# Performance work log

Hardware: AMD Instinct MI355X
Metric: run time of the kernel (lower is better)

## Reference

```python
import jax, jax.numpy as jnp
import numpy as np

V, E, H, T, B, L = 50000, 256, 256, 20, 64, 512
START, STOP = 18, 19
NEG = -10000.0


def setup_inputs() -> dict:
    key = jax.random.key(0)
    ks = jax.random.split(key, 16)
    lengths = jnp.sort(jax.random.randint(ks[0], (B,), 1, L + 1))[::-1]
    lengths = lengths.at[0].set(L)  # pack_padded requires sorted descending
    sentences = jax.random.randint(ks[1], (B, L), 0, V)
    s = lambda k, shp, sc: jax.random.normal(k, shp, jnp.float32) * sc
    trans = jax.random.normal(ks[12], (T, T), jnp.float32)
    trans = trans.at[START, :].set(NEG).at[:, STOP].set(NEG)
    return {
        "sentences": sentences,
        "lengths": lengths,
        "emb": s(ks[2], (V, E), 1.0),
        "w_ih_f": s(ks[3], (4 * H, E), 0.05),
        "w_hh_f": s(ks[4], (4 * H, H), 0.05),
        "b_ih_f": s(ks[5], (4 * H,), 0.05),
        "b_hh_f": s(ks[6], (4 * H,), 0.05),
        "w_ih_b": s(ks[7], (4 * H, E), 0.05),
        "w_hh_b": s(ks[8], (4 * H, H), 0.05),
        "b_ih_b": s(ks[9], (4 * H,), 0.05),
        "b_hh_b": s(ks[10], (4 * H,), 0.05),
        "w_out": s(ks[11], (T, 2 * H), 0.05),
        "b_out": s(ks[13], (T,), 0.05),
        "transitions": trans,
    }


def _lstm(x, mask, w_ih, w_hh, b_ih, b_hh):
    # x: [B,L,E]; mask: [B,L] bool. Masked scan == packed-sequence LSTM
    # (hidden frozen past length, outputs zero past length like pad_packed).
    h0 = jnp.zeros((x.shape[0], H), x.dtype)
    bias = b_ih + b_hh

    def step(carry, inp):
        h, c = carry
        xt, mt = inp
        g = xt @ w_ih.T + h @ w_hh.T + bias
        i, f, gg, o = jnp.split(g, 4, axis=-1)  # torch gate order i,f,g,o
        c_new = jax.nn.sigmoid(f) * c + jax.nn.sigmoid(i) * jnp.tanh(gg)
        h_new = jax.nn.sigmoid(o) * jnp.tanh(c_new)
        m = mt[:, None]
        h = jnp.where(m, h_new, h)
        c = jnp.where(m, c_new, c)
        return (h, c), jnp.where(m, h_new, 0.0)

    _, hs = jax.lax.scan(step, (h0, h0), (x.transpose(1, 0, 2), mask.T))
    return hs.transpose(1, 0, 2)  # [B,L,H]


def _emissions(sentences, lengths, emb, w_ih_f, w_hh_f, b_ih_f, b_hh_f,
               w_ih_b, w_hh_b, b_ih_b, b_hh_b, w_out, b_out):
    mask = jnp.arange(L)[None, :] < lengths[:, None]  # [B,L]
    embeds = emb[sentences]  # [B,L,E]
    out_f = _lstm(embeds, mask, w_ih_f, w_hh_f, b_ih_f, b_hh_f)
    # backward dir: reverse each sequence within its own length
    rev_idx = jnp.clip(lengths[:, None] - 1 - jnp.arange(L)[None, :], 0, L - 1)
    x_rev = jnp.take_along_axis(embeds, rev_idx[:, :, None], axis=1)
    h_rev = _lstm(x_rev, mask, w_ih_b, w_hh_b, b_ih_b, b_hh_b)
    out_b = jnp.take_along_axis(h_rev, rev_idx[:, :, None], axis=1) * mask[..., None]
    lstm_out = jnp.concatenate([out_f, out_b], axis=-1)  # [B,L,2H]
    return lstm_out @ w_out.T + b_out  # [B,L,T]


def _viterbi(scores, lengths, transitions):
    mask = jnp.arange(L)[None, :] < lengths[:, None]
    fv0 = jnp.full((B, T), NEG, scores.dtype).at[:, START].set(0.0)

    def step(fv, inp):
        sc_t, m_t = inp  # [B,T], [B]
        ntv = fv[:, None, :] + transitions[None]  # [B,T(next),T(prev)]
        best = jnp.argmax(ntv, axis=-1)
        fv_new = jnp.max(ntv, axis=-1) + sc_t
        fv = jnp.where(m_t[:, None], fv_new, fv)
        bp = jnp.where(m_t[:, None], best, STOP)
        return fv, bp

    fv, bps = jax.lax.scan(step, fv0, (scores.transpose(1, 0, 2), mask.T))
    terminal = fv + transitions[STOP][None, :]  # [B,T]
    last_best = jnp.argmax(terminal, axis=-1)  # [B]
    path_scores = jnp.take_along_axis(terminal, last_best[:, None], axis=1)[:, 0]

    # backtrace: j runs L-1..1; writes tag for position j-1 when j < length
    barange = jnp.arange(B)

    def back(cur, j):
        valid = j < lengths
        new = jnp.where(valid, bps[j, barange, cur], cur)
        return new, new

    js = jnp.arange(L - 1, 0, -1)
    _, tags_rev = jax.lax.scan(back, last_best, js)  # [L-1,B]
    tags = tags_rev[::-1].T  # [B,L-1], positions 0..L-2
    pos = jnp.arange(L)[None, :]
    paths = jnp.where(pos < (lengths - 1)[:, None],
                      jnp.pad(tags, ((0, 0), (0, 1))), 0)
    paths = paths.at[barange, lengths - 1].set(last_best)  # pad past length with 0
    return path_scores, paths


def reference(sentences, lengths, emb, w_ih_f, w_hh_f, b_ih_f, b_hh_f,
              w_ih_b, w_hh_b, b_ih_b, b_hh_b, w_out, b_out, transitions):
    scores = _emissions(sentences, lengths, emb, w_ih_f, w_hh_f, b_ih_f, b_hh_f,
                        w_ih_b, w_hh_b, b_ih_b, b_hh_b, w_out, b_out)
    path_scores, paths = _viterbi(scores, lengths, transitions)
    return path_scores, paths
```

## Files before the change

### kernel.cpp

```cpp
#include <hip/hip_runtime.h>
#include <hip/hip_bf16.h>
#include <math.h>

#define NV 50000
#define NE 256
#define NH 256
#define NT 20
#define NB 64
#define NL 512
#define TAG_START 18
#define TAG_STOP 19
#define NEGV -10000.0f

typedef unsigned short ushortT;
typedef __attribute__((ext_vector_type(4))) float f32x4;
typedef __attribute__((ext_vector_type(8))) short short8;
typedef __attribute__((ext_vector_type(4))) unsigned short us4;

#define PINV(x) asm volatile("" : "+v"(x))

__device__ __forceinline__ float sigf_slow(float x) { return 1.0f / (1.0f + expf(-x)); }
__device__ __forceinline__ float fsig(float x) { return 1.0f / (1.0f + __expf(-x)); }
__device__ __forceinline__ float ftanh(float x) { return 1.0f - 2.0f / (1.0f + __expf(2.0f * x)); }
__device__ __forceinline__ ushortT f2bf(float f) {
    unsigned int u = __float_as_uint(f);
    u += 0x7fffu + ((u >> 16) & 1u);
    return (ushortT)(u >> 16);
}
__device__ __forceinline__ float bf2f(unsigned int bits16) {
    return __uint_as_float(bits16 << 16);
}


__global__ __launch_bounds__(256) void k_cvtw(
    const float* __restrict__ whh_f, const float* __restrict__ whh_b,
    const float* __restrict__ wih_f, const float* __restrict__ wih_b,
    ushortT* __restrict__ whh16, ushortT* __restrict__ wih16)
{
    int idx = blockIdx.x * 256 + threadIdx.x;
    const float* s; ushortT* d;
    switch (blockIdx.y) {
        case 0: s = whh_f; d = whh16;            break;
        case 1: s = whh_b; d = whh16 + 262144;   break;
        case 2: s = wih_f; d = wih16;            break;
        default: s = wih_b; d = wih16 + 262144;  break;
    }
    d[idx] = f2bf(s[idx]);
}

__global__ __launch_bounds__(1024) void k_bias(
    const float* __restrict__ bih_f, const float* __restrict__ bhh_f,
    const float* __restrict__ bih_b, const float* __restrict__ bhh_b,
    float* __restrict__ biasc)
{
    int n = threadIdx.x;
    if (blockIdx.x == 0) biasc[n] = bih_f[n] + bhh_f[n];
    else                 biasc[1024 + n] = bih_b[n] + bhh_b[n];
}

__global__
__attribute__((amdgpu_flat_work_group_size(512, 512)))
__attribute__((amdgpu_waves_per_eu(2, 2)))
void k_gin_mfma(
    const int* __restrict__ sent, const int* __restrict__ lens,
    const float* __restrict__ emb, const ushortT* __restrict__ wih16,
    const float* __restrict__ biasc, ushortT* __restrict__ gin16,
    int chunk_start, int CH)
{
    const int g = blockIdx.x, tsub = blockIdx.y;
    const int dir = blockIdx.z >> 1, half = blockIdx.z & 1;
    const int gmax = lens[g * 16];
    const int tt0 = tsub * 16;
    if (chunk_start + tt0 >= gmax) return;

    const int tid = threadIdx.x;
    const int w = tid >> 6, l = tid & 63, lr = l & 15, lg = l >> 4;

    __shared__ char x_raw[16 * 512];

    const int ucol = half * 128 + w * 16 + lr;
    short8 bfr[4][8];
    float bias_l[4];
    const ushortT* wsrc = wih16 + dir * 262144;
#pragma unroll
    for (int nt = 0; nt < 4; ++nt) {
        int col = nt * 256 + ucol;
        bias_l[nt] = biasc[dir * 1024 + col];
#pragma unroll
        for (int kt = 0; kt < 8; ++kt)
            bfr[nt][kt] = *(const short8*)(wsrc + (size_t)col * 256 + kt * 32 + lg * 8);
    }
#pragma unroll
    for (int nt = 0; nt < 4; ++nt) {
        PINV(bias_l[nt]);
#pragma unroll
        for (int kt = 0; kt < 8; ++kt) PINV(bfr[nt][kt]);
    }

    const int srow = tid >> 5, sseg = tid & 31;
    const int slen = lens[g * 16 + srow];
    const int sb = (g * 16 + srow) * 512;

    for (int i = 0; i < 16; ++i) {
        int tg = chunk_start + tt0 + i;
        if (tg >= gmax) break;

        int tsrc = dir ? (slen - 1 - tg) : tg;
        if (tsrc < 0) tsrc = 0;
        if (tsrc > 511) tsrc = 511;
        int tok = sent[sb + tsrc];
        const float* es = emb + (size_t)tok * 256 + sseg * 8;
        float4 e0 = *(const float4*)es;
        float4 e1 = *(const float4*)(es + 4);
        short8 xv;
        xv[0] = (short)f2bf(e0.x); xv[1] = (short)f2bf(e0.y);
        xv[2] = (short)f2bf(e0.z); xv[3] = (short)f2bf(e0.w);
        xv[4] = (short)f2bf(e1.x); xv[5] = (short)f2bf(e1.y);
        xv[6] = (short)f2bf(e1.z); xv[7] = (short)f2bf(e1.w);
        int sa = (srow * 512 + sseg * 16) ^ ((srow & 7) << 4);
        *(short8*)&x_raw[sa] = xv;
        __syncthreads();

        short8 af[8];
#pragma unroll
        for (int kt = 0; kt < 8; ++kt) {
            int a = (lr * 512 + kt * 64 + lg * 16) ^ ((lr & 7) << 4);
            af[kt] = *(const short8*)&x_raw[a];
        }
        f32x4 acc[4];
#pragma unroll
        for (int nt = 0; nt < 4; ++nt) {
            acc[nt][0] = bias_l[nt]; acc[nt][1] = bias_l[nt];
            acc[nt][2] = bias_l[nt]; acc[nt][3] = bias_l[nt];
        }
#pragma unroll
        for (int kt = 0; kt < 8; ++kt)
#pragma unroll
            for (int nt = 0; nt < 4; ++nt)
                acc[nt] = __builtin_amdgcn_mfma_f32_16x16x32_bf16(af[kt], bfr[nt][kt], acc[nt], 0, 0, 0);

        ushortT* gp = gin16 + ((size_t)((dir * 4 + g) * CH + (tt0 + i))) * 16384;
#pragma unroll
        for (int nt = 0; nt < 4; ++nt) {
            int col = nt * 256 + ucol;
            us4 st;
            st[0] = f2bf(acc[nt][0]); st[1] = f2bf(acc[nt][1]);
            st[2] = f2bf(acc[nt][2]); st[3] = f2bf(acc[nt][3]);
            *(us4*)(gp + col * 16 + lg * 4) = st;
        }
        __syncthreads();
    }
}

__global__
__attribute__((amdgpu_flat_work_group_size(512, 512)))
__attribute__((amdgpu_waves_per_eu(2, 2)))
void k_rec_mfma(
    const int* __restrict__ lens, const ushortT* __restrict__ whh16,
    const ushortT* __restrict__ gin16, ushortT* __restrict__ hout,
    ushortT* __restrict__ st_h, float* __restrict__ st_c,
    unsigned int* __restrict__ hexu, unsigned int* __restrict__ flags,
    int chunk_start, int CH)
{
    const int bid = blockIdx.x;
    const int half = bid >> 3;
    const int dirg = bid & 7;
    const int g = dirg & 3, dir = dirg >> 2;
    const int gmax = lens[g * 16];
    const int nsteps = min(CH, gmax - chunk_start);
    if (nsteps <= 0) return;

    const int tid = threadIdx.x;
    const int w = tid >> 6, l = tid & 63, lr = l & 15, lg = l >> 4;

    __shared__ char h_s[2][8192];

    int lenr[4];
#pragma unroll
    for (int r = 0; r < 4; ++r) lenr[r] = lens[g * 16 + lg * 4 + r];

    const int ucol = half * 128 + w * 16 + lr;
    short8 bfr[4][8];
    {
        const ushortT* wsrc = whh16 + dir * 262144;
#pragma unroll
        for (int nt = 0; nt < 4; ++nt) {
            const ushortT* wp = wsrc + (size_t)(nt * 256 + ucol) * 256 + lg * 8;
#pragma unroll
            for (int kt = 0; kt < 8; ++kt)
                bfr[nt][kt] = *(const short8*)(wp + kt * 32);
        }
    }

    float c[4];
    if (chunk_start == 0) {
#pragma unroll
        for (int r = 0; r < 4; ++r) c[r] = 0.0f;
        for (int i = tid; i < 2048; i += 512) ((int*)h_s[0])[i] = 0;
    } else {
        const float* cs = st_c + ((size_t)(dirg * 2 + half)) * 2048 + tid * 4;
#pragma unroll
        for (int r = 0; r < 4; ++r) c[r] = cs[r];
        const int* hs = (const int*)st_h + dirg * 2048;
        for (int i = tid; i < 2048; i += 512) ((int*)h_s[0])[i] = hs[i];
    }
    __syncthreads();

    unsigned int* exu = hexu + dirg * 4096;
    unsigned int* flagMe = flags + dirg * 32 + half * 16;
    unsigned int* flagPeer = flags + dirg * 32 + (half ^ 1) * 16;

    const int pub_base = ucol * 8 + lg * 2;

    int pf_uidx[2], pf_lds0[2], pf_lds1[2];
#pragma unroll
    for (int s2 = 0; s2 < 2; ++s2) {
        int i = tid * 2 + s2;
        int pcol = ((half ^ 1) << 7) + (i >> 3);
        int sub = i & 7;
        pf_uidx[s2] = pcol * 8 + sub;
        int r0 = (sub >> 1) * 4 + (sub & 1) * 2;
        pf_lds0[s2] = (r0 * 512 + pcol * 2) ^ ((r0 & 7) << 4);
        int r1 = r0 + 1;
        pf_lds1[s2] = (r1 * 512 + pcol * 2) ^ ((r1 & 7) << 4);
    }

    const ushortT* ginp = gin16 + (size_t)dirg * CH * 16384;
    int p = 0;
    for (int tt = 0; tt < nsteps; ++tt) {
        const int t_glob = chunk_start + tt;

        const ushortT* gb = ginp + (size_t)tt * 16384 + lg * 4;
        us4 gv[4];
#pragma unroll
        for (int nt = 0; nt < 4; ++nt)
            gv[nt] = *(const us4*)(gb + (nt * 256 + ucol) * 16);

        const char* hb = h_s[p];
        f32x4 acc[4];
#pragma unroll
        for (int nt = 0; nt < 4; ++nt) { acc[nt][0] = 0.f; acc[nt][1] = 0.f; acc[nt][2] = 0.f; acc[nt][3] = 0.f; }
#pragma unroll
        for (int kt = 0; kt < 8; ++kt) {
            int a_ = (lr * 512 + kt * 64 + lg * 16) ^ ((lr & 7) << 4);
            short8 af = *(const short8*)&hb[a_];
#pragma unroll
            for (int nt = 0; nt < 4; ++nt)
                acc[nt] = __builtin_amdgcn_mfma_f32_16x16x32_bf16(af, bfr[nt][kt], acc[nt], 0, 0, 0);
        }

        char* hw = h_s[p ^ 1];
        unsigned int* exs = exu + ((t_glob + 1) & 1) * 2048;
        ushortT hh[4];
#pragma unroll
        for (int r = 0; r < 4; ++r) {
            float i_ = acc[0][r] + bf2f(gv[0][r]);
            float f_ = acc[1][r] + bf2f(gv[1][r]);
            float g_ = acc[2][r] + bf2f(gv[2][r]);
            float o_ = acc[3][r] + bf2f(gv[3][r]);
            float cn = fsig(f_) * c[r] + fsig(i_) * ftanh(g_);
            float hn = fsig(o_) * ftanh(cn);
            c[r] = cn;
            hh[r] = f2bf(hn);
            int row = lg * 4 + r;
            *(ushortT*)&hw[(row * 512 + ucol * 2) ^ ((row & 7) << 4)] = hh[r];
        }
        unsigned int v01 = (unsigned int)hh[0] | ((unsigned int)hh[1] << 16);
        unsigned int v23 = (unsigned int)hh[2] | ((unsigned int)hh[3] << 16);
        __hip_atomic_store(&exs[pub_base + 0], v01, __ATOMIC_RELAXED, __HIP_MEMORY_SCOPE_AGENT);
        __hip_atomic_store(&exs[pub_base + 1], v23, __ATOMIC_RELAXED, __HIP_MEMORY_SCOPE_AGENT);

        __syncthreads();

        if (tid == 0)
            __hip_atomic_store(flagMe, (unsigned int)(t_glob + 1), __ATOMIC_RELEASE, __HIP_MEMORY_SCOPE_AGENT);

#pragma unroll
        for (int r = 0; r < 4; ++r) {
            if (t_glob < lenr[r]) {
                int row = lg * 4 + r;
                int tp = dir ? (lenr[r] - 1 - t_glob) : t_glob;
                hout[((size_t)((g * 16 + row) * 512 + tp)) * 512 + dir * 256 + ucol] = hh[r];
            }
        }

        {
            unsigned int tgt = (unsigned int)(t_glob + 1);
            int guard = 0;
            while (__hip_atomic_load(flagPeer, __ATOMIC_RELAXED, __HIP_MEMORY_SCOPE_AGENT) < tgt
                   && ++guard < (1 << 16)) {}
        }

#pragma unroll
        for (int s2 = 0; s2 < 2; ++s2) {
            unsigned int v = __hip_atomic_load(&exs[pf_uidx[s2]], __ATOMIC_RELAXED, __HIP_MEMORY_SCOPE_AGENT);
            *(ushortT*)&hw[pf_lds0[s2]] = (ushortT)(v & 0xffffu);
            *(ushortT*)&hw[pf_lds1[s2]] = (ushortT)(v >> 16);
        }
        __syncthreads();
        p ^= 1;
    }

    float* cs = st_c + ((size_t)(dirg * 2 + half)) * 2048 + tid * 4;
#pragma unroll
    for (int r = 0; r < 4; ++r) cs[r] = c[r];
    if (half == 0) {
        int* hs = (int*)st_h + dirg * 2048;
        for (int i = tid; i < 2048; i += 512) hs[i] = ((int*)h_s[p])[i];
    }
}

__global__ __launch_bounds__(256) void k_scores_bf(
    const int* __restrict__ lens, const ushortT* __restrict__ hout,
    const float* __restrict__ w_out, const float* __restrict__ b_out,
    float* __restrict__ scores)
{
    const int b = blockIdx.y;
    const int t0 = blockIdx.x * 32;
    const int len = lens[b];
    if (t0 >= len) return;

    __shared__ float w_s[20 * 513];
    __shared__ float row_s[512];
    __shared__ float part_s[20][9];
    __shared__ float bo_s[20];

    const int tid = threadIdx.x;
    for (int e = tid; e < 20 * 512; e += 256) w_s[(e >> 9) * 513 + (e & 511)] = w_out[e];
    if (tid < 20) bo_s[tid] = b_out[tid];
    __syncthreads();

    const int tend = min(t0 + 32, len);
    const int tag = tid >> 3, sl = tid & 7;
    for (int t = t0; t < tend; ++t) {
        const ushortT* hr = hout + ((size_t)(b * 512 + t)) * 512;
        unsigned int v = ((const unsigned int*)hr)[tid];
        row_s[tid * 2] = bf2f(v & 0xffffu);
        row_s[tid * 2 + 1] = bf2f(v >> 16);
        __syncthreads();
        if (tid < 160) {
            float s = 0.0f;
#pragma unroll 8
            for (int j = 0; j < 64; ++j) {
                int k = sl + (((j + tag) & 63) << 3);
                s = fmaf(w_s[tag * 513 + k], row_s[k], s);
            }
            part_s[tag][sl] = s;
        }
        __syncthreads();
        if (tid < 20) {
            float s = bo_s[tid];
#pragma unroll
            for (int j = 0; j < 8; ++j) s += part_s[tid][j];
            scores[((size_t)(b * 512 + t)) * 20 + tid] = s;
        }
        __syncthreads();
    }
}

__global__ __launch_bounds__(64) void k_viterbi_s(
    const int* __restrict__ lens, const float* __restrict__ scores,
    const float* __restrict__ trans, float* __restrict__ out)
{
    const int b = blockIdx.x;
    const int lane = threadIdx.x;
    const int len = lens[b];

    __shared__ float tr_s[20][21];
    __shared__ float fv_s[20];
    __shared__ float term_s[20];
    __shared__ unsigned char bp_s[512][20];
    __shared__ unsigned char path_s[512];

    for (int e = lane; e < 400; e += 64) tr_s[e / 20][e % 20] = trans[e];
    if (lane < 20) fv_s[lane] = (lane == TAG_START) ? 0.0f : NEGV;
    __syncthreads();

    const float* sc = scores + ((size_t)(b << 9)) * 20;
    for (int t = 0; t < len; ++t) {
        float m = 0.0f; int arg = 0;
        if (lane < 20) {
            m = fv_s[0] + tr_s[lane][0]; arg = 0;
#pragma unroll
            for (int k = 1; k < 20; ++k) {
                float v = fv_s[k] + tr_s[lane][k];
                if (v > m) { m = v; arg = k; }
            }
            m += sc[t * 20 + lane];
        }
        __syncthreads();
        if (lane < 20) { fv_s[lane] = m; bp_s[t][lane] = (unsigned char)arg; }
        __syncthreads();
    }

    if (lane < 20) term_s[lane] = fv_s[lane] + tr_s[TAG_STOP][lane];
    __syncthreads();

    if (lane == 0) {
        float m = term_s[0]; int arg = 0;
        for (int k = 1; k < 20; ++k) if (term_s[k] > m) { m = term_s[k]; arg = k; }
        out[b] = m;
        int cur = arg;
        path_s[len - 1] = (unsigned char)cur;
        for (int j = len - 1; j >= 1; --j) {
            cur = bp_s[j][cur];
            path_s[j - 1] = (unsigned char)cur;
        }
    }
    __syncthreads();

    float* po = out + NB + ((size_t)b << 9);
    for (int p = lane; p < NL; p += 64) po[p] = (p < len) ? (float)path_s[p] : 0.0f;
}

__global__ __launch_bounds__(256) void k_transpose_fb(
    const float* __restrict__ whh_f, const float* __restrict__ whh_b,
    const float* __restrict__ wih_f, const float* __restrict__ wih_b,
    float* __restrict__ thh_f, float* __restrict__ thh_b,
    float* __restrict__ tih_f, float* __restrict__ tih_b)
{
    int e = blockIdx.x * 256 + threadIdx.x;
    const float* wm; float* wt;
    switch (blockIdx.y) {
        case 0: wm = whh_f; wt = thh_f; break;
        case 1: wm = whh_b; wt = thh_b; break;
        case 2: wm = wih_f; wt = tih_f; break;
        default: wm = wih_b; wt = tih_b; break;
    }
    int n = e >> 8, k = e & 255;
    wt[k * 1024 + n] = wm[e];
}

__global__ __launch_bounds__(1024) void k_rec_fb(
    const int* __restrict__ sent, const int* __restrict__ lens,
    const float* __restrict__ emb,
    const float* __restrict__ thh_f, const float* __restrict__ thh_b,
    const float* __restrict__ tih_f, const float* __restrict__ tih_b,
    const float* __restrict__ b_ih_f, const float* __restrict__ b_hh_f,
    const float* __restrict__ b_ih_b, const float* __restrict__ b_hh_b,
    const float* __restrict__ w_out,
    float* __restrict__ sc_f, float* __restrict__ sc_b)
{
    const int b = blockIdx.x, dir = blockIdx.y;
    const int len = lens[b];
    const int n = threadIdx.x;
    const float* Whh = dir ? thh_b : thh_f;
    const float* Wih = dir ? tih_b : tih_f;
    const float* bi = dir ? b_ih_b : b_ih_f;
    const float* bh = dir ? b_hh_b : b_hh_f;
    float* scout = dir ? sc_b : sc_f;

    __shared__ float x_s[256];
    __shared__ float h_s[256];
    __shared__ float g_s[1024];
    __shared__ float bias_s[1024];
    __shared__ float wout_s[20 * 257];
    __shared__ float part_s[20][8];

    bias_s[n] = bi[n] + bh[n];
    for (int e = n; e < 20 * 256; e += 1024)
        wout_s[(e >> 8) * 257 + (e & 255)] = w_out[(e >> 8) * 512 + dir * 256 + (e & 255)];
    if (n < 256) h_s[n] = 0.0f;
    float c = 0.0f;
    __syncthreads();

    const int sbase = b << 9;
    for (int t = 0; t < len; ++t) {
        if (n < 256) {
            int ti = dir ? (len - 1 - t) : t;
            int tok = sent[sbase + ti];
            x_s[n] = emb[(size_t)tok * NE + n];
        }
        __syncthreads();
        float acc = bias_s[n];
        const float* wi = Wih + n;
        const float* wh = Whh + n;
#pragma unroll 8
        for (int k = 0; k < 256; ++k) {
            acc = fmaf(wh[(size_t)(k << 10)], h_s[k], acc);
            acc = fmaf(wi[(size_t)(k << 10)], x_s[k], acc);
        }
        g_s[n] = acc;
        __syncthreads();
        if (n < 256) {
            float ig = g_s[n], fg = g_s[n + 256], gg = g_s[n + 512], og = g_s[n + 768];
            float cn = sigf_slow(fg) * c + sigf_slow(ig) * tanhf(gg);
            float hn = sigf_slow(og) * tanhf(cn);
            c = cn; h_s[n] = hn;
        }
        __syncthreads();
        if (n < 160) {
            const int tag = n >> 3, sl = n & 7;
            const float* wrow = wout_s + tag * 257;
            float s = 0.0f;
#pragma unroll 8
            for (int j = 0; j < 32; ++j) { int k = sl + (j << 3); s = fmaf(wrow[k], h_s[k], s); }
            part_s[tag][sl] = s;
        }
        __syncthreads();
        if (n < 20) {
            float s = part_s[n][0];
#pragma unroll
            for (int j = 1; j < 8; ++j) s += part_s[n][j];
            int tp = dir ? (len - 1 - t) : t;
            scout[(size_t)(sbase + tp) * 20 + n] = s;
        }
    }
}

__global__ __launch_bounds__(64) void k_viterbi_fb(
    const int* __restrict__ lens,
    const float* __restrict__ sc_f, const float* __restrict__ sc_b,
    const float* __restrict__ b_out, const float* __restrict__ trans,
    float* __restrict__ out)
{
    const int b = blockIdx.x;
    const int lane = threadIdx.x;
    const int len = lens[b];

    __shared__ float tr_s[20][21];
    __shared__ float fv_s[20];
    __shared__ float term_s[20];
    __shared__ float bo_s[20];
    __shared__ unsigned char bp_s[512][20];
    __shared__ unsigned char path_s[512];

    for (int e = lane; e < 400; e += 64) tr_s[e / 20][e % 20] = trans[e];
    if (lane < 20) { fv_s[lane] = (lane == TAG_START) ? 0.0f : NEGV; bo_s[lane] = b_out[lane]; }
    __syncthreads();

    const size_t sb = (size_t)(b << 9) * 20;
    for (int t = 0; t < len; ++t) {
        float m = 0.0f; int arg = 0;
        if (lane < 20) {
            m = fv_s[0] + tr_s[lane][0]; arg = 0;
#pragma unroll
            for (int k = 1; k < 20; ++k) {
                float v = fv_s[k] + tr_s[lane][k];
                if (v > m) { m = v; arg = k; }
            }
            m += sc_f[sb + t * 20 + lane] + sc_b[sb + t * 20 + lane] + bo_s[lane];
        }
        __syncthreads();
        if (lane < 20) { fv_s[lane] = m; bp_s[t][lane] = (unsigned char)arg; }
        __syncthreads();
    }
    if (lane < 20) term_s[lane] = fv_s[lane] + tr_s[TAG_STOP][lane];
    __syncthreads();
    if (lane == 0) {
        float m = term_s[0]; int arg = 0;
        for (int k = 1; k < 20; ++k) if (term_s[k] > m) { m = term_s[k]; arg = k; }
        out[b] = m;
        int cur = arg;
        path_s[len - 1] = (unsigned char)cur;
        for (int j = len - 1; j >= 1; --j) { cur = bp_s[j][cur]; path_s[j - 1] = (unsigned char)cur; }
    }
    __syncthreads();
    float* po = out + NB + ((size_t)b << 9);
    for (int p = lane; p < NL; p += 64) po[p] = (p < len) ? (float)path_s[p] : 0.0f;
}

extern "C" void kernel_launch(void* const* d_in, const int* in_sizes, int n_in,
                              void* d_out, int out_size, void* d_ws, size_t ws_size,
                              hipStream_t stream)
{
    const int*   sent   = (const int*)d_in[0];
    const int*   lens   = (const int*)d_in[1];
    const float* emb    = (const float*)d_in[2];
    const float* w_ih_f = (const float*)d_in[3];
    const float* w_hh_f = (const float*)d_in[4];
    const float* b_ih_f = (const float*)d_in[5];
    const float* b_hh_f = (const float*)d_in[6];
    const float* w_ih_b = (const float*)d_in[7];
    const float* w_hh_b = (const float*)d_in[8];
    const float* b_ih_b = (const float*)d_in[9];
    const float* b_hh_b = (const float*)d_in[10];
    const float* w_out  = (const float*)d_in[11];
    const float* b_out  = (const float*)d_in[12];
    const float* trans  = (const float*)d_in[13];
    float* out = (float*)d_out;

    char* w = (char*)d_ws;
    const size_t base = 38612992;
    int CH = 0;
    const int chs[6] = {512, 256, 192, 128, 64, 32};
    for (int i = 0; i < 6; ++i)
        if (base + (size_t)chs[i] * 262144 <= ws_size) { CH = chs[i]; break; }

    if (CH) {
        ushortT* whh16 = (ushortT*)(w);
        ushortT* wih16 = (ushortT*)(w + 1048576);
        float*   biasc = (float*)(w + 2097152);
        ushortT* st_h  = (ushortT*)(w + 2105344);
        float*   st_c  = (float*)(w + 2170880);
        unsigned int* hexu = (unsigned int*)(w + 2301952);
        unsigned int* flags = (unsigned int*)(w + 2433024);
        float*   scores= (float*)(w + 2437120);
        ushortT* hout  = (ushortT*)(w + 5058560);
        ushortT* gin16 = (ushortT*)(w + base);

        hipMemsetAsync(flags, 0, 4096, stream);
        k_cvtw<<<dim3(1024, 4), 256, 0, stream>>>(w_hh_f, w_hh_b, w_ih_f, w_ih_b, whh16, wih16);
        k_bias<<<2, 1024, 0, stream>>>(b_ih_f, b_hh_f, b_ih_b, b_hh_b, biasc);

        for (int cs = 0; cs < NL; cs += CH) {
            k_gin_mfma<<<dim3(4, CH / 16, 4), 512, 0, stream>>>(
                sent, lens, emb, wih16, biasc, gin16, cs, CH);
            k_rec_mfma<<<dim3(16), 512, 0, stream>>>(
                lens, whh16, gin16, hout, st_h, st_c, hexu, flags, cs, CH);
        }
        k_scores_bf<<<dim3(16, 64), 256, 0, stream>>>(lens, hout, w_out, b_out, scores);
        k_viterbi_s<<<64, 64, 0, stream>>>(lens, scores, trans, out);
    } else {
        float* ws2   = (float*)d_ws;
        float* thh_f = ws2;
        float* thh_b = thh_f + 262144;
        float* tih_f = thh_b + 262144;
        float* tih_b = tih_f + 262144;
        float* sc_f  = tih_b + 262144;
        float* sc_b  = sc_f + (size_t)NB * NL * NT;

        k_transpose_fb<<<dim3(1024, 4), 256, 0, stream>>>(
            w_hh_f, w_hh_b, w_ih_f, w_ih_b, thh_f, thh_b, tih_f, tih_b);
        k_rec_fb<<<dim3(NB, 2), 1024, 0, stream>>>(
            sent, lens, emb, thh_f, thh_b, tih_f, tih_b,
            b_ih_f, b_hh_f, b_ih_b, b_hh_b, w_out, sc_f, sc_b);
        k_viterbi_fb<<<NB, 64, 0, stream>>>(lens, sc_f, sc_b, b_out, trans, out);
    }
}
```

Measured before the change: 2.131 ms.

## Process two batch groups per recurrence block, halving block count

Each recurrent LSTM block now handles two 16-row batch groups (A and B) that share the same register-resident W_hh fragments, instead of one group per block. The grid shrinks from 16 to 8 blocks. The aim is to interleave two independent recurrences so MFMA, gate math and cross-block exchange latency for one group overlap with the other, and to cut the per-step barrier and handshake cost per unit of work. In exchange each block does roughly twice the per-step work on the serial critical path. Fewer blocks also means less of the GPU is used in parallel.

New measurement: 3.315 ms. 1.56x slower.

```diff
diff --git a/kernel.cpp b/kernel.cpp
--- a/kernel.cpp
+++ b/kernel.cpp
@@ -163,21 +163,27 @@
     int chunk_start, int CH)
 {
     const int bid = blockIdx.x;
-    const int half = bid >> 3;
-    const int dirg = bid & 7;
-    const int g = dirg & 3, dir = dirg >> 2;
-    const int gmax = lens[g * 16];
-    const int nsteps = min(CH, gmax - chunk_start);
-    if (nsteps <= 0) return;
+    const int half = bid >> 2;
+    const int dgp = bid & 3;
+    const int dir = dgp >> 1, gp = dgp & 1;
+    const int gA = gp * 2, gB = gp * 2 + 1;
+    const int dirgA = dir * 4 + gA, dirgB = dir * 4 + gB;
+    const int nA = min(CH, lens[gA * 16] - chunk_start);
+    const int nB = min(CH, lens[gB * 16] - chunk_start);
+    if (nA <= 0) return;
 
     const int tid = threadIdx.x;
     const int w = tid >> 6, l = tid & 63, lr = l & 15, lg = l >> 4;
 
-    __shared__ char h_s[2][8192];
-
-    int lenr[4];
-#pragma unroll
-    for (int r = 0; r < 4; ++r) lenr[r] = lens[g * 16 + lg * 4 + r];
+    __shared__ char h_sA[2][8192];
+    __shared__ char h_sB[2][8192];
+
+    int lenrA[4], lenrB[4];
+#pragma unroll
+    for (int r = 0; r < 4; ++r) {
+        lenrA[r] = lens[gA * 16 + lg * 4 + r];
+        lenrB[r] = lens[gB * 16 + lg * 4 + r];
+    }
 
     const int ucol = half * 128 + w * 16 + lr;
     short8 bfr[4][8];
@@ -192,23 +198,34 @@
         }
     }
 
-    float c[4];
+    float cA[4], cB[4];
     if (chunk_start == 0) {
 #pragma unroll
-        for (int r = 0; r < 4; ++r) c[r] = 0.0f;
-        for (int i = tid; i < 2048; i += 512) ((int*)h_s[0])[i] = 0;
+        for (int r = 0; r < 4; ++r) { cA[r] = 0.0f; cB[r] = 0.0f; }
+        for (int i = tid; i < 2048; i += 512) {
+            ((int*)h_sA[0])[i] = 0;
+            ((int*)h_sB[0])[i] = 0;
+        }
     } else {
-        const float* cs = st_c + ((size_t)(dirg * 2 + half)) * 2048 + tid * 4;
-#pragma unroll
-        for (int r = 0; r < 4; ++r) c[r] = cs[r];
-        const int* hs = (const int*)st_h + dirg * 2048;
-        for (int i = tid; i < 2048; i += 512) ((int*)h_s[0])[i] = hs[i];
-    }
-    __syncthreads();
-
-    unsigned int* exu = hexu + dirg * 4096;
-    unsigned int* flagMe = flags + dirg * 32 + half * 16;
-    unsigned int* flagPeer = flags + dirg * 32 + (half ^ 1) * 16;
+        const float* csA = st_c + ((size_t)(dirgA * 2 + half)) * 2048 + tid * 4;
+        const float* csB = st_c + ((size_t)(dirgB * 2 + half)) * 2048 + tid * 4;
+#pragma unroll
+        for (int r = 0; r < 4; ++r) { cA[r] = csA[r]; cB[r] = csB[r]; }
+        const int* hsA = (const int*)st_h + dirgA * 2048;
+        const int* hsB = (const int*)st_h + dirgB * 2048;
+        for (int i = tid; i < 2048; i += 512) {
+            ((int*)h_sA[0])[i] = hsA[i];
+            ((int*)h_sB[0])[i] = hsB[i];
+        }
+    }
+    __syncthreads();
+
+    unsigned int* exuA = hexu + dirgA * 4096;
+    unsigned int* exuB = hexu + dirgB * 4096;
+    unsigned int* flagMeA   = flags + dirgA * 32 + half * 16;
+    unsigned int* flagPeerA = flags + dirgA * 32 + (half ^ 1) * 16;
+    unsigned int* flagMeB   = flags + dirgB * 32 + half * 16;
+    unsigned int* flagPeerB = flags + dirgB * 32 + (half ^ 1) * 16;
 
     const int pub_base = ucol * 8 + lg * 2;
 
@@ -225,88 +242,170 @@
         pf_lds1[s2] = (r1 * 512 + pcol * 2) ^ ((r1 & 7) << 4);
     }
 
-    const ushortT* ginp = gin16 + (size_t)dirg * CH * 16384;
-    int p = 0;
-    for (int tt = 0; tt < nsteps; ++tt) {
+    const ushortT* ginpA = gin16 + (size_t)dirgA * CH * 16384;
+    const ushortT* ginpB = gin16 + (size_t)dirgB * CH * 16384;
+
+    int pA = 0, pB = 0;
+    for (int tt = 0; tt < nA; ++tt) {
         const int t_glob = chunk_start + tt;
-
-        const ushortT* gb = ginp + (size_t)tt * 16384 + lg * 4;
-        us4 gv[4];
-#pragma unroll
-        for (int nt = 0; nt < 4; ++nt)
-            gv[nt] = *(const us4*)(gb + (nt * 256 + ucol) * 16);
-
-        const char* hb = h_s[p];
-        f32x4 acc[4];
-#pragma unroll
-        for (int nt = 0; nt < 4; ++nt) { acc[nt][0] = 0.f; acc[nt][1] = 0.f; acc[nt][2] = 0.f; acc[nt][3] = 0.f; }
-#pragma unroll
-        for (int kt = 0; kt < 8; ++kt) {
-            int a_ = (lr * 512 + kt * 64 + lg * 16) ^ ((lr & 7) << 4);
-            short8 af = *(const short8*)&hb[a_];
+        const bool doB = (tt < nB);
+        ushortT hhA[4], hhB[4];
+
+        {
+            const ushortT* gb = ginpA + (size_t)tt * 16384 + lg * 4;
+            us4 gv[4];
 #pragma unroll
             for (int nt = 0; nt < 4; ++nt)
-                acc[nt] = __builtin_amdgcn_mfma_f32_16x16x32_bf16(af, bfr[nt][kt], acc[nt], 0, 0, 0);
-        }
-
-        char* hw = h_s[p ^ 1];
-        unsigned int* exs = exu + ((t_glob + 1) & 1) * 2048;
-        ushortT hh[4];
+                gv[nt] = *(const us4*)(gb + (nt * 256 + ucol) * 16);
+
+            const char* hb = h_sA[pA];
+            f32x4 acc[4];
+#pragma unroll
+            for (int nt = 0; nt < 4; ++nt) { acc[nt][0] = 0.f; acc[nt][1] = 0.f; acc[nt][2] = 0.f; acc[nt][3] = 0.f; }
+#pragma unroll
+            for (int kt = 0; kt < 8; ++kt) {
+                int a_ = (lr * 512 + kt * 64 + lg * 16) ^ ((lr & 7) << 4);
+                short8 af = *(const short8*)&hb[a_];
+#pragma unroll
+                for (int nt = 0; nt < 4; ++nt)
+                    acc[nt] = __builtin_amdgcn_mfma_f32_16x16x32_bf16(af, bfr[nt][kt], acc[nt], 0, 0, 0);
+            }
+
+            char* hw = h_sA[pA ^ 1];
+            unsigned int* exs = exuA + ((t_glob + 1) & 1) * 2048;
+#pragma unroll
+            for (int r = 0; r < 4; ++r) {
+                float i_ = acc[0][r] + bf2f(gv[0][r]);
+                float f_ = acc[1][r] + bf2f(gv[1][r]);
+                float g_ = acc[2][r] + bf2f(gv[2][r]);
+                float o_ = acc[3][r] + bf2f(gv[3][r]);
+                float cn = fsig(f_) * cA[r] + fsig(i_) * ftanh(g_);
+                float hn = fsig(o_) * ftanh(cn);
+                cA[r] = cn;
+                hhA[r] = f2bf(hn);
+                int row = lg * 4 + r;
+                *(ushortT*)&hw[(row * 512 + ucol * 2) ^ ((row & 7) << 4)] = hhA[r];
+            }
+            unsigned int v01 = (unsigned int)hhA[0] | ((unsigned int)hhA[1] << 16);
+            unsigned int v23 = (unsigned int)hhA[2] | ((unsigned int)hhA[3] << 16);
+            __hip_atomic_store(&exs[pub_base + 0], v01, __ATOMIC_RELAXED, __HIP_MEMORY_SCOPE_AGENT);
+            __hip_atomic_store(&exs[pub_base + 1], v23, __ATOMIC_RELAXED, __HIP_MEMORY_SCOPE_AGENT);
+        }
+
+        if (doB) {
+            const ushortT* gb = ginpB + (size_t)tt * 16384 + lg * 4;
+            us4 gv[4];
+#pragma unroll
+            for (int nt = 0; nt < 4; ++nt)
+                gv[nt] = *(const us4*)(gb + (nt * 256 + ucol) * 16);
+
+            const char* hb = h_sB[pB];
+            f32x4 acc[4];
+#pragma unroll
+            for (int nt = 0; nt < 4; ++nt) { acc[nt][0] = 0.f; acc[nt][1] = 0.f; acc[nt][2] = 0.f; acc[nt][3] = 0.f; }
+#pragma unroll
+            for (int kt = 0; kt < 8; ++kt) {
+                int a_ = (lr * 512 + kt * 64 + lg * 16) ^ ((lr & 7) << 4);
+                short8 af = *(const short8*)&hb[a_];
+#pragma unroll
+                for (int nt = 0; nt < 4; ++nt)
+                    acc[nt] = __builtin_amdgcn_mfma_f32_16x16x32_bf16(af, bfr[nt][kt], acc[nt], 0, 0, 0);
+            }
+
+            char* hw = h_sB[pB ^ 1];
+            unsigned int* exs = exuB + ((t_glob + 1) & 1) * 2048;
+#pragma unroll
+            for (int r = 0; r < 4; ++r) {
+                float i_ = acc[0][r] + bf2f(gv[0][r]);
+                float f_ = acc[1][r] + bf2f(gv[1][r]);
+                float g_ = acc[2][r] + bf2f(gv[2][r]);
+                float o_ = acc[3][r] + bf2f(gv[3][r]);
+                float cn = fsig(f_) * cB[r] + fsig(i_) * ftanh(g_);
+                float hn = fsig(o_) * ftanh(cn);
+                cB[r] = cn;
+                hhB[r] = f2bf(hn);
+                int row = lg * 4 + r;
+                *(ushortT*)&hw[(row * 512 + ucol * 2) ^ ((row & 7) << 4)] = hhB[r];
+            }
+            unsigned int v01 = (unsigned int)hhB[0] | ((unsigned int)hhB[1] << 16);
+            unsigned int v23 = (unsigned int)hhB[2] | ((unsigned int)hhB[3] << 16);
+            __hip_atomic_store(&exs[pub_base + 0], v01, __ATOMIC_RELAXED, __HIP_MEMORY_SCOPE_AGENT);
+            __hip_atomic_store(&exs[pub_base + 1], v23, __ATOMIC_RELAXED, __HIP_MEMORY_SCOPE_AGENT);
+        }
+
+        __syncthreads();
+
+        if (tid == 0) {
+            __hip_atomic_store(flagMeA, (unsigned int)(t_glob + 1), __ATOMIC_RELEASE, __HIP_MEMORY_SCOPE_AGENT);
+            if (doB)
+                __hip_atomic_store(flagMeB, (unsigned int)(t_glob + 1), __ATOMIC_RELEASE, __HIP_MEMORY_SCOPE_AGENT);
+        }
+
 #pragma unroll
         for (int r = 0; r < 4; ++r) {
-            float i_ = acc[0][r] + bf2f(gv[0][r]);
-            float f_ = acc[1][r] + bf2f(gv[1][r]);
-            float g_ = acc[2][r] + bf2f(gv[2][r]);
-            float o_ = acc[3][r] + bf2f(gv[3][r]);
-            float cn = fsig(f_) * c[r] + fsig(i_) * ftanh(g_);
-            float hn = fsig(o_) * ftanh(cn);
-            c[r] = cn;
-            hh[r] = f2bf(hn);
-            int row = lg * 4 + r;
-            *(ushortT*)&hw[(row * 512 + ucol * 2) ^ ((row & 7) << 4)] = hh[r];
-        }
-        unsigned int v01 = (unsigned int)hh[0] | ((unsigned int)hh[1] << 16);
-        unsigned int v23 = (unsigned int)hh[2] | ((unsigned int)hh[3] << 16);
-        __hip_atomic_store(&exs[pub_base + 0], v01, __ATOMIC_RELAXED, __HIP_MEMORY_SCOPE_AGENT);
-        __hip_atomic_store(&exs[pub_base + 1], v23, __ATOMIC_RELAXED, __HIP_MEMORY_SCOPE_AGENT);
-
-        __syncthreads();
-
-        if (tid == 0)
-            __hip_atomic_store(flagMe, (unsigned int)(t_glob + 1), __ATOMIC_RELEASE, __HIP_MEMORY_SCOPE_AGENT);
-
-#pragma unroll
-        for (int r = 0; r < 4; ++r) {
-            if (t_glob < lenr[r]) {
+            if (t_glob < lenrA[r]) {
                 int row = lg * 4 + r;
-                int tp = dir ? (lenr[r] - 1 - t_glob) : t_glob;
-                hout[((size_t)((g * 16 + row) * 512 + tp)) * 512 + dir * 256 + ucol] = hh[r];
+                int tp = dir ? (lenrA[r] - 1 - t_glob) : t_glob;
+                hout[((size_t)((gA * 16 + row) * 512 + tp)) * 512 + dir * 256 + ucol] = hhA[r];
+            }
+        }
+        if (doB) {
+#pragma unroll
+            for (int r = 0; r < 4; ++r) {
+                if (t_glob < lenrB[r]) {
+                    int row = lg * 4 + r;
+                    int tp = dir ? (lenrB[r] - 1 - t_glob) : t_glob;
+                    hout[((size_t)((gB * 16 + row) * 512 + tp)) * 512 + dir * 256 + ucol] = hhB[r];
+                }
             }
         }
 
         {
             unsigned int tgt = (unsigned int)(t_glob + 1);
             int guard = 0;
-            while (__hip_atomic_load(flagPeer, __ATOMIC_RELAXED, __HIP_MEMORY_SCOPE_AGENT) < tgt
+            while (__hip_atomic_load(flagPeerA, __ATOMIC_RELAXED, __HIP_MEMORY_SCOPE_AGENT) < tgt
                    && ++guard < (1 << 16)) {}
-        }
-
-#pragma unroll
-        for (int s2 = 0; s2 < 2; ++s2) {
-            unsigned int v = __hip_atomic_load(&exs[pf_uidx[s2]], __ATOMIC_RELAXED, __HIP_MEMORY_SCOPE_AGENT);
-            *(ushortT*)&hw[pf_lds0[s2]] = (ushortT)(v & 0xffffu);
-            *(ushortT*)&hw[pf_lds1[s2]] = (ushortT)(v >> 16);
-        }
-        __syncthreads();
-        p ^= 1;
-    }
-
-    float* cs = st_c + ((size_t)(dirg * 2 + half)) * 2048 + tid * 4;
-#pragma unroll
-    for (int r = 0; r < 4; ++r) cs[r] = c[r];
-    if (half == 0) {
-        int* hs = (int*)st_h + dirg * 2048;
-        for (int i = tid; i < 2048; i += 512) hs[i] = ((int*)h_s[p])[i];
+            unsigned int* exs = exuA + (tgt & 1) * 2048;
+            char* hw = h_sA[pA ^ 1];
+#pragma unroll
+            for (int s2 = 0; s2 < 2; ++s2) {
+                unsigned int v = __hip_atomic_load(&exs[pf_uidx[s2]], __ATOMIC_RELAXED, __HIP_MEMORY_SCOPE_AGENT);
+                *(ushortT*)&hw[pf_lds0[s2]] = (ushortT)(v & 0xffffu);
+                *(ushortT*)&hw[pf_lds1[s2]] = (ushortT)(v >> 16);
+            }
+        }
+        if (doB) {
+            unsigned int tgt = (unsigned int)(t_glob + 1);
+            int guard = 0;
+            while (__hip_atomic_load(flagPeerB, __ATOMIC_RELAXED, __HIP_MEMORY_SCOPE_AGENT) < tgt
+                   && ++guard < (1 << 16)) {}
+            unsigned int* exs = exuB + (tgt & 1) * 2048;
+            char* hw = h_sB[pB ^ 1];
+#pragma unroll
+            for (int s2 = 0; s2 < 2; ++s2) {
+                unsigned int v = __hip_atomic_load(&exs[pf_uidx[s2]], __ATOMIC_RELAXED, __HIP_MEMORY_SCOPE_AGENT);
+                *(ushortT*)&hw[pf_lds0[s2]] = (ushortT)(v & 0xffffu);
+                *(ushortT*)&hw[pf_lds1[s2]] = (ushortT)(v >> 16);
+            }
+        }
+        __syncthreads();
+        pA ^= 1;
+        if (doB) pB ^= 1;
+    }
+
+    {
+        float* csA = st_c + ((size_t)(dirgA * 2 + half)) * 2048 + tid * 4;
+        float* csB = st_c + ((size_t)(dirgB * 2 + half)) * 2048 + tid * 4;
+#pragma unroll
+        for (int r = 0; r < 4; ++r) { csA[r] = cA[r]; csB[r] = cB[r]; }
+        if (half == 0) {
+            int* hsA = (int*)st_h + dirgA * 2048;
+            int* hsB = (int*)st_h + dirgB * 2048;
+            for (int i = tid; i < 2048; i += 512) {
+                hsA[i] = ((int*)h_sA[pA])[i];
+                hsB[i] = ((int*)h_sB[pB])[i];
+            }
+        }
     }
 }
 
@@ -606,7 +705,7 @@
         for (int cs = 0; cs < NL; cs += CH) {
             k_gin_mfma<<<dim3(4, CH / 16, 4), 512, 0, stream>>>(
                 sent, lens, emb, wih16, biasc, gin16, cs, CH);
-            k_rec_mfma<<<dim3(16), 512, 0, stream>>>(
+            k_rec_mfma<<<dim3(8), 512, 0, stream>>>(
                 lens, whh16, gin16, hout, st_h, st_c, hexu, flags, cs, CH);
         }
         k_scores_bf<<<dim3(16, 64), 256, 0, stream>>>(lens, hout, w_out, b_out, scores);
```
